# Kernel optimization log

Measured on AMD Instinct MI355X. Metric: run time of the kernel, lower is better.

## Reference

```python
import jax, jax.numpy as jnp
import numpy as np

DEPTH = 6
IN_FEATURES = 256
NUM_TREES = 256
TREE_DIM = 1
BATCH = 2048


def sparsemax(X, axis=0):
    """Full-sort sparsemax projection along `axis` (k=None path of the torch code)."""
    X = jnp.moveaxis(X, axis, -1)
    Xs = X - jnp.max(X, axis=-1, keepdims=True)
    z = -jnp.sort(-Xs, axis=-1)                      # descending sort
    cs = jnp.cumsum(z, axis=-1) - 1.0                # topk_cumsum - 1
    d = X.shape[-1]
    rho = jnp.arange(1, d + 1, dtype=X.dtype)
    support = rho * z > cs
    k = jnp.sum(support, axis=-1, keepdims=True)     # support size (int)
    tau = jnp.take_along_axis(cs, k - 1, axis=-1) / k.astype(X.dtype)
    out = jnp.maximum(Xs - tau, 0.0)
    return jnp.moveaxis(out, -1, axis)


def sparsemoid(x):
    return jnp.clip(0.5 * x + 0.5, 0.0, 1.0)


def bin_codes_1hot(depth, dtype=jnp.float32):
    idx = jnp.arange(2 ** depth)
    off = 2 ** jnp.arange(depth)
    codes = ((idx[None, :] // off[:, None]) % 2).astype(dtype)   # [depth, 2^depth]
    return jnp.stack([codes, 1.0 - codes], axis=-1)              # [depth, 2^depth, 2]


def setup_inputs() -> dict:
    key = jax.random.key(0)
    k1, k2, k3, k4, k5 = jax.random.split(key, 5)
    x = jax.random.normal(k1, (BATCH, IN_FEATURES), dtype=jnp.float32)
    response = jax.random.normal(k2, (NUM_TREES, TREE_DIM, 2 ** DEPTH), dtype=jnp.float32)
    feature_selection_logits = jax.random.uniform(k3, (IN_FEATURES, NUM_TREES, DEPTH), dtype=jnp.float32)
    feature_thresholds = 0.5 * jax.random.normal(k4, (NUM_TREES, DEPTH), dtype=jnp.float32)
    log_temperatures = jnp.zeros((NUM_TREES, DEPTH), dtype=jnp.float32)
    return {
        "x": x,
        "response": response,
        "feature_selection_logits": feature_selection_logits,
        "feature_thresholds": feature_thresholds,
        "log_temperatures": log_temperatures,
    }


def reference(x, response, feature_selection_logits, feature_thresholds, log_temperatures):
    depth = feature_thresholds.shape[-1]
    codes = bin_codes_1hot(depth, x.dtype)                          # [d, 2^d, 2]
    # sparsemax feature routing over the feature axis
    fs = sparsemax(feature_selection_logits, axis=0)                # [F, T, d]
    fv = jnp.einsum('bi,ind->bnd', x, fs)                           # [B, T, d]
    tl = (fv - feature_thresholds) * jnp.exp(-log_temperatures)     # [B, T, d]
    bins = sparsemoid(jnp.stack([-tl, tl], axis=-1))                # [B, T, d, 2]
    bin_matches = jnp.einsum('btds,dcs->btdc', bins, codes)         # [B, T, d, 2^d]
    response_weights = jnp.prod(bin_matches, axis=-2)               # [B, T, 2^d]
    out = jnp.einsum('bnd,ncd->bnc', response_weights, response)    # [B, T, C]
    return out.reshape(out.shape[0], -1)                            # flatten_output=True
```

## Files before the change

kernel.cpp:

```cpp
#include <hip/hip_runtime.h>
#include <math.h>

#define NF 256
#define NT 256
#define ND 6
#define NB 2048
#define NCOL (NT * ND)
#define NLEAF 64

typedef __attribute__((ext_vector_type(8))) short bf16x8;
typedef __attribute__((ext_vector_type(4))) float f32x4;
typedef __attribute__((ext_vector_type(8))) unsigned short u16x8;

__device__ inline unsigned short f2bf(float f) {
    unsigned u = __float_as_uint(f);
    u += 0x7fffu + ((u >> 16) & 1u);
    return (unsigned short)(u >> 16);
}
__device__ inline float bf2f(unsigned short h) {
    return __uint_as_float(((unsigned)h) << 16);
}

__global__ __launch_bounds__(256) void convert_x_kernel(
    const float* __restrict__ x,
    unsigned short* __restrict__ xh,
    unsigned short* __restrict__ xl)
{
    const int i = (blockIdx.x * 256 + threadIdx.x) * 4;
    const float4 v = *(const float4*)&x[i];
    const unsigned short h0 = f2bf(v.x), h1 = f2bf(v.y), h2 = f2bf(v.z), h3 = f2bf(v.w);
    *(ushort4*)&xh[i] = make_ushort4(h0, h1, h2, h3);
    *(ushort4*)&xl[i] = make_ushort4(f2bf(v.x - bf2f(h0)), f2bf(v.y - bf2f(h1)),
                                     f2bf(v.z - bf2f(h2)), f2bf(v.w - bf2f(h3)));
}

__global__ __launch_bounds__(256) void sparsemax_kernel(
    const float* __restrict__ fsl,
    unsigned short* __restrict__ fs_hi,
    unsigned short* __restrict__ fs_lo)
{
    __shared__ float s[NF];
    __shared__ int wk[4];
    const int col = blockIdx.x;
    const int tid = threadIdx.x;

    const float v = fsl[tid * NCOL + col];

    s[tid] = v;
    __syncthreads();
    for (int off = 128; off > 0; off >>= 1) {
        if (tid < off) s[tid] = fmaxf(s[tid], s[tid + off]);
        __syncthreads();
    }
    const float xmax = s[0];
    __syncthreads();

    const float xs = v - xmax;

    s[tid] = xs;
    __syncthreads();
    for (int k = 2; k <= NF; k <<= 1) {
        for (int j = k >> 1; j > 0; j >>= 1) {
            const int ixj = tid ^ j;
            if (ixj > tid) {
                const float a = s[tid];
                const float b = s[ixj];
                const bool desc = ((tid & k) == 0);
                if (desc ? (a < b) : (a > b)) { s[tid] = b; s[ixj] = a; }
            }
            __syncthreads();
        }
    }
    const float z = s[tid];

    for (int off = 1; off < NF; off <<= 1) {
        const float tmp = (tid >= off) ? s[tid - off] : 0.0f;
        __syncthreads();
        s[tid] += tmp;
        __syncthreads();
    }

    const bool flag = ((float)(tid + 1) * z > s[tid] - 1.0f);
    const unsigned long long m = __ballot(flag);
    if ((tid & 63) == 0) wk[tid >> 6] = __popcll(m);
    __syncthreads();
    const int k = wk[0] + wk[1] + wk[2] + wk[3];

    const float tau = (s[k - 1] - 1.0f) / (float)k;
    const float val = fmaxf(xs - tau, 0.0f);
    const unsigned short h = f2bf(val);
    fs_hi[col * NF + tid] = h;
    fs_lo[col * NF + tid] = f2bf(val - bf2f(h));
}

#define TM 64
#define TN 64
#define TK 32

__global__ __launch_bounds__(256) void gemm_mfma_kernel(
    const unsigned short* __restrict__ Ah, const unsigned short* __restrict__ Al,
    const unsigned short* __restrict__ Bh, const unsigned short* __restrict__ Bl,
    float* __restrict__ C)
{
    __shared__ unsigned short sAh[TM][TK], sAl[TM][TK];
    __shared__ unsigned short sBh[TN][TK], sBl[TN][TK];

    const int tid  = threadIdx.x;
    const int lane = tid & 63;
    const int w    = tid >> 6;
    const int wm   = w & 1;
    const int wn   = w >> 1;
    const int bm0  = blockIdx.y * TM;
    const int bn0  = blockIdx.x * TN;

    const int l15  = lane & 15;
    const int quad = lane >> 4;

    const int srow  = tid >> 2;
    const int skseg = (tid & 3) * 8;

    f32x4 acc[2][2] = {};

    for (int k0 = 0; k0 < NF; k0 += TK) {
        *(u16x8*)&sAh[srow][skseg] = *(const u16x8*)&Ah[(bm0 + srow) * NF + k0 + skseg];
        *(u16x8*)&sAl[srow][skseg] = *(const u16x8*)&Al[(bm0 + srow) * NF + k0 + skseg];
        *(u16x8*)&sBh[srow][skseg] = *(const u16x8*)&Bh[(bn0 + srow) * NF + k0 + skseg];
        *(u16x8*)&sBl[srow][skseg] = *(const u16x8*)&Bl[(bn0 + srow) * NF + k0 + skseg];
        __syncthreads();

        #pragma unroll
        for (int im = 0; im < 2; im++) {
            const bf16x8 a_h = *(const bf16x8*)&sAh[wm * 32 + im * 16 + l15][quad * 8];
            const bf16x8 a_l = *(const bf16x8*)&sAl[wm * 32 + im * 16 + l15][quad * 8];
            #pragma unroll
            for (int in = 0; in < 2; in++) {
                const bf16x8 b_h = *(const bf16x8*)&sBh[wn * 32 + in * 16 + l15][quad * 8];
                const bf16x8 b_l = *(const bf16x8*)&sBl[wn * 32 + in * 16 + l15][quad * 8];
                acc[im][in] = __builtin_amdgcn_mfma_f32_16x16x32_bf16(a_h, b_h, acc[im][in], 0, 0, 0);
                acc[im][in] = __builtin_amdgcn_mfma_f32_16x16x32_bf16(a_h, b_l, acc[im][in], 0, 0, 0);
                acc[im][in] = __builtin_amdgcn_mfma_f32_16x16x32_bf16(a_l, b_h, acc[im][in], 0, 0, 0);
            }
        }
        __syncthreads();
    }

    #pragma unroll
    for (int im = 0; im < 2; im++)
        #pragma unroll
        for (int in = 0; in < 2; in++)
            #pragma unroll
            for (int r = 0; r < 4; r++) {
                const int m = bm0 + wm * 32 + im * 16 + quad * 4 + r;
                const int n = bn0 + wn * 32 + in * 16 + l15;
                C[m * NCOL + n] = acc[im][in][r];
            }
}

__global__ __launch_bounds__(256) void tree_kernel(
    const float* __restrict__ fv,
    const float* __restrict__ thr,
    const float* __restrict__ ltemp,
    const float* __restrict__ resp,
    float* __restrict__ out)
{
    const int b = blockIdx.x;
    const int t = threadIdx.x;

    float sp[ND], sm[ND];
    #pragma unroll
    for (int d = 0; d < ND; d++) {
        const float f  = fv[b * NCOL + t * ND + d];
        const float tl = (f - thr[t * ND + d]) * expf(-ltemp[t * ND + d]);
        const float h  = 0.5f * tl;
        sp[d] = fminf(fmaxf(0.5f + h, 0.0f), 1.0f);
        sm[d] = fminf(fmaxf(0.5f - h, 0.0f), 1.0f);
    }

    float wleaf[NLEAF];
    wleaf[0] = 1.0f;
    #pragma unroll
    for (int d = 0; d < ND; d++) {
        const int half = 1 << d;
        #pragma unroll
        for (int c = 0; c < NLEAF / 2; c++) {
            if (c < half) {
                const float base = wleaf[c];
                wleaf[c + half] = base * sm[d];
                wleaf[c]        = base * sp[d];
            }
        }
    }

    float acc = 0.0f;
    #pragma unroll
    for (int c = 0; c < NLEAF; c++)
        acc = fmaf(wleaf[c], resp[t * NLEAF + c], acc);

    out[b * NT + t] = acc;
}

extern "C" void kernel_launch(void* const* d_in, const int* in_sizes, int n_in,
                              void* d_out, int out_size, void* d_ws, size_t ws_size,
                              hipStream_t stream)
{
    const float* x    = (const float*)d_in[0];
    const float* resp = (const float*)d_in[1];
    const float* fsl  = (const float*)d_in[2];
    const float* thr  = (const float*)d_in[3];
    const float* lt   = (const float*)d_in[4];
    float* out = (float*)d_out;

    float* fv = (float*)d_ws;
    unsigned short* xh    = (unsigned short*)(fv + (size_t)NB * NCOL);
    unsigned short* xl    = xh + (size_t)NB * NF;
    unsigned short* fs_hi = xl + (size_t)NB * NF;
    unsigned short* fs_lo = fs_hi + (size_t)NCOL * NF;

    convert_x_kernel<<<NB * NF / (256 * 4), 256, 0, stream>>>(x, xh, xl);
    sparsemax_kernel<<<NCOL, 256, 0, stream>>>(fsl, fs_hi, fs_lo);

    dim3 g(NCOL / TN, NB / TM);
    gemm_mfma_kernel<<<g, 256, 0, stream>>>(xh, xl, fs_hi, fs_lo, fv);

    tree_kernel<<<NB, 256, 0, stream>>>(fv, thr, lt, resp, out);
}
```

Baseline: 110.8 us.

## Fuse GEMM with tree epilogue, inline x conversion, use Michelot sparsemax

Replaces the sort-based sparsemax with a per-wavefront Michelot fixed-point iteration that handles four columns per block using shuffles. The x bf16 hi/lo split moves into the GEMM tile load. The tree evaluation becomes a GEMM epilogue working from shared memory, with N tiles widened to 96 so each tile covers 16 whole trees. This removes two kernel launches and the global round trip of the 2048x1536 feature-value matrix. In exchange it adds an iterative sparsemax whose iteration count depends on the data, and a heavier epilogue per block.

```diff
diff --git a/kernel.cpp b/kernel.cpp
--- a/kernel.cpp
+++ b/kernel.cpp
@@ -21,89 +21,84 @@
     return __uint_as_float(((unsigned)h) << 16);
 }
 
-__global__ __launch_bounds__(256) void convert_x_kernel(
-    const float* __restrict__ x,
-    unsigned short* __restrict__ xh,
-    unsigned short* __restrict__ xl)
-{
-    const int i = (blockIdx.x * 256 + threadIdx.x) * 4;
-    const float4 v = *(const float4*)&x[i];
-    const unsigned short h0 = f2bf(v.x), h1 = f2bf(v.y), h2 = f2bf(v.z), h3 = f2bf(v.w);
-    *(ushort4*)&xh[i] = make_ushort4(h0, h1, h2, h3);
-    *(ushort4*)&xl[i] = make_ushort4(f2bf(v.x - bf2f(h0)), f2bf(v.y - bf2f(h1)),
-                                     f2bf(v.z - bf2f(h2)), f2bf(v.w - bf2f(h3)));
-}
-
-__global__ __launch_bounds__(256) void sparsemax_kernel(
+__global__ __launch_bounds__(256) void sparsemax_michelot(
     const float* __restrict__ fsl,
     unsigned short* __restrict__ fs_hi,
     unsigned short* __restrict__ fs_lo)
 {
-    __shared__ float s[NF];
-    __shared__ int wk[4];
-    const int col = blockIdx.x;
-    const int tid = threadIdx.x;
-
-    const float v = fsl[tid * NCOL + col];
-
-    s[tid] = v;
-    __syncthreads();
-    for (int off = 128; off > 0; off >>= 1) {
-        if (tid < off) s[tid] = fmaxf(s[tid], s[tid + off]);
-        __syncthreads();
-    }
-    const float xmax = s[0];
-    __syncthreads();
-
-    const float xs = v - xmax;
-
-    s[tid] = xs;
-    __syncthreads();
-    for (int k = 2; k <= NF; k <<= 1) {
-        for (int j = k >> 1; j > 0; j >>= 1) {
-            const int ixj = tid ^ j;
-            if (ixj > tid) {
-                const float a = s[tid];
-                const float b = s[ixj];
-                const bool desc = ((tid & k) == 0);
-                if (desc ? (a < b) : (a > b)) { s[tid] = b; s[ixj] = a; }
-            }
-            __syncthreads();
-        }
-    }
-    const float z = s[tid];
-
-    for (int off = 1; off < NF; off <<= 1) {
-        const float tmp = (tid >= off) ? s[tid - off] : 0.0f;
-        __syncthreads();
-        s[tid] += tmp;
-        __syncthreads();
-    }
-
-    const bool flag = ((float)(tid + 1) * z > s[tid] - 1.0f);
-    const unsigned long long m = __ballot(flag);
-    if ((tid & 63) == 0) wk[tid >> 6] = __popcll(m);
-    __syncthreads();
-    const int k = wk[0] + wk[1] + wk[2] + wk[3];
-
-    const float tau = (s[k - 1] - 1.0f) / (float)k;
-    const float val = fmaxf(xs - tau, 0.0f);
-    const unsigned short h = f2bf(val);
-    fs_hi[col * NF + tid] = h;
-    fs_lo[col * NF + tid] = f2bf(val - bf2f(h));
+    const int lane = threadIdx.x & 63;
+    const int col  = blockIdx.x * 4 + (threadIdx.x >> 6);
+
+    float x[4];
+    #pragma unroll
+    for (int j = 0; j < 4; j++)
+        x[j] = fsl[(lane + 64 * j) * NCOL + col];
+
+    float mx = fmaxf(fmaxf(x[0], x[1]), fmaxf(x[2], x[3]));
+    #pragma unroll
+    for (int off = 32; off > 0; off >>= 1)
+        mx = fmaxf(mx, __shfl_xor(mx, off));
+    #pragma unroll
+    for (int j = 0; j < 4; j++) x[j] -= mx;
+
+    float s = (x[0] + x[1]) + (x[2] + x[3]);
+    #pragma unroll
+    for (int off = 32; off > 0; off >>= 1)
+        s += __shfl_xor(s, off);
+    float tau = (s - 1.0f) / 256.0f;
+
+    int prev = 256;
+    for (int it = 0; it < 64; it++) {
+        float ss = 0.0f, cc = 0.0f;
+        #pragma unroll
+        for (int j = 0; j < 4; j++)
+            if (x[j] > tau) { ss += x[j]; cc += 1.0f; }
+        #pragma unroll
+        for (int off = 32; off > 0; off >>= 1) {
+            ss += __shfl_xor(ss, off);
+            cc += __shfl_xor(cc, off);
+        }
+        const int c = (int)cc;
+        if (c == prev) break;
+        prev = c;
+        tau = (ss - 1.0f) / cc;
+    }
+
+    #pragma unroll
+    for (int j = 0; j < 4; j++) {
+        const float v = fmaxf(x[j] - tau, 0.0f);
+        const unsigned short h = f2bf(v);
+        fs_hi[col * NF + lane + 64 * j] = h;
+        fs_lo[col * NF + lane + 64 * j] = f2bf(v - bf2f(h));
+    }
 }
 
 #define TM 64
-#define TN 64
+#define TN 96
 #define TK 32
-
-__global__ __launch_bounds__(256) void gemm_mfma_kernel(
-    const unsigned short* __restrict__ Ah, const unsigned short* __restrict__ Al,
-    const unsigned short* __restrict__ Bh, const unsigned short* __restrict__ Bl,
-    float* __restrict__ C)
+#define PK (TK + 8)
+
+union SMem {
+    struct {
+        unsigned short Ah[TM][PK], Al[TM][PK];
+        unsigned short Bh[TN][PK], Bl[TN][PK];
+    } st;
+    struct {
+        float fv[TM][TN + 1];
+        float resp[16][NLEAF];
+    } ep;
+};
+
+__global__ __launch_bounds__(256) void gemm_tree_kernel(
+    const float* __restrict__ x,
+    const unsigned short* __restrict__ Bh,
+    const unsigned short* __restrict__ Bl,
+    const float* __restrict__ thr,
+    const float* __restrict__ ltemp,
+    const float* __restrict__ resp_g,
+    float* __restrict__ out)
 {
-    __shared__ unsigned short sAh[TM][TK], sAl[TM][TK];
-    __shared__ unsigned short sBh[TN][TK], sBl[TN][TK];
+    __shared__ SMem sm;
 
     const int tid  = threadIdx.x;
     const int lane = tid & 63;
@@ -112,30 +107,54 @@
     const int wn   = w >> 1;
     const int bm0  = blockIdx.y * TM;
     const int bn0  = blockIdx.x * TN;
+    const int t0   = blockIdx.x * 16;
 
     const int l15  = lane & 15;
     const int quad = lane >> 4;
 
-    const int srow  = tid >> 2;
-    const int skseg = (tid & 3) * 8;
-
-    f32x4 acc[2][2] = {};
+    const int arow  = tid >> 2;
+    const int akseg = (tid & 3) * 8;
+    const int bhalf = tid >> 7;
+    const int brow  = (tid & 127) >> 2;
+    const int bkseg = (tid & 3) * 8;
+
+    f32x4 acc[2][3] = {};
 
     for (int k0 = 0; k0 < NF; k0 += TK) {
-        *(u16x8*)&sAh[srow][skseg] = *(const u16x8*)&Ah[(bm0 + srow) * NF + k0 + skseg];
-        *(u16x8*)&sAl[srow][skseg] = *(const u16x8*)&Al[(bm0 + srow) * NF + k0 + skseg];
-        *(u16x8*)&sBh[srow][skseg] = *(const u16x8*)&Bh[(bn0 + srow) * NF + k0 + skseg];
-        *(u16x8*)&sBl[srow][skseg] = *(const u16x8*)&Bl[(bn0 + srow) * NF + k0 + skseg];
+        {
+            const float4 v0 = *(const float4*)&x[(bm0 + arow) * NF + k0 + akseg];
+            const float4 v1 = *(const float4*)&x[(bm0 + arow) * NF + k0 + akseg + 4];
+            const float vv[8] = {v0.x, v0.y, v0.z, v0.w, v1.x, v1.y, v1.z, v1.w};
+            u16x8 hi, lo;
+            #pragma unroll
+            for (int j = 0; j < 8; j++) {
+                const unsigned short h = f2bf(vv[j]);
+                hi[j] = h;
+                lo[j] = f2bf(vv[j] - bf2f(h));
+            }
+            *(u16x8*)&sm.st.Ah[arow][akseg] = hi;
+            *(u16x8*)&sm.st.Al[arow][akseg] = lo;
+        }
+        {
+            const unsigned short* __restrict__ src = bhalf ? Bl : Bh;
+            unsigned short (*dst)[PK] = bhalf ? sm.st.Bl : sm.st.Bh;
+            #pragma unroll
+            for (int c = 0; c < 3; c++) {
+                const int row = c * 32 + brow;
+                *(u16x8*)&dst[row][bkseg] =
+                    *(const u16x8*)&src[(bn0 + row) * NF + k0 + bkseg];
+            }
+        }
         __syncthreads();
 
         #pragma unroll
         for (int im = 0; im < 2; im++) {
-            const bf16x8 a_h = *(const bf16x8*)&sAh[wm * 32 + im * 16 + l15][quad * 8];
-            const bf16x8 a_l = *(const bf16x8*)&sAl[wm * 32 + im * 16 + l15][quad * 8];
-            #pragma unroll
-            for (int in = 0; in < 2; in++) {
-                const bf16x8 b_h = *(const bf16x8*)&sBh[wn * 32 + in * 16 + l15][quad * 8];
-                const bf16x8 b_l = *(const bf16x8*)&sBl[wn * 32 + in * 16 + l15][quad * 8];
+            const bf16x8 a_h = *(const bf16x8*)&sm.st.Ah[wm * 32 + im * 16 + l15][quad * 8];
+            const bf16x8 a_l = *(const bf16x8*)&sm.st.Al[wm * 32 + im * 16 + l15][quad * 8];
+            #pragma unroll
+            for (int in = 0; in < 3; in++) {
+                const bf16x8 b_h = *(const bf16x8*)&sm.st.Bh[wn * 48 + in * 16 + l15][quad * 8];
+                const bf16x8 b_l = *(const bf16x8*)&sm.st.Bl[wn * 48 + in * 16 + l15][quad * 8];
                 acc[im][in] = __builtin_amdgcn_mfma_f32_16x16x32_bf16(a_h, b_h, acc[im][in], 0, 0, 0);
                 acc[im][in] = __builtin_amdgcn_mfma_f32_16x16x32_bf16(a_h, b_l, acc[im][in], 0, 0, 0);
                 acc[im][in] = __builtin_amdgcn_mfma_f32_16x16x32_bf16(a_l, b_h, acc[im][in], 0, 0, 0);
@@ -147,56 +166,59 @@
     #pragma unroll
     for (int im = 0; im < 2; im++)
         #pragma unroll
-        for (int in = 0; in < 2; in++)
+        for (int in = 0; in < 3; in++)
             #pragma unroll
             for (int r = 0; r < 4; r++) {
-                const int m = bm0 + wm * 32 + im * 16 + quad * 4 + r;
-                const int n = bn0 + wn * 32 + in * 16 + l15;
-                C[m * NCOL + n] = acc[im][in][r];
-            }
-}
-
-__global__ __launch_bounds__(256) void tree_kernel(
-    const float* __restrict__ fv,
-    const float* __restrict__ thr,
-    const float* __restrict__ ltemp,
-    const float* __restrict__ resp,
-    float* __restrict__ out)
-{
-    const int b = blockIdx.x;
-    const int t = threadIdx.x;
-
-    float sp[ND], sm[ND];
-    #pragma unroll
-    for (int d = 0; d < ND; d++) {
-        const float f  = fv[b * NCOL + t * ND + d];
-        const float tl = (f - thr[t * ND + d]) * expf(-ltemp[t * ND + d]);
-        const float h  = 0.5f * tl;
-        sp[d] = fminf(fmaxf(0.5f + h, 0.0f), 1.0f);
-        sm[d] = fminf(fmaxf(0.5f - h, 0.0f), 1.0f);
-    }
-
-    float wleaf[NLEAF];
-    wleaf[0] = 1.0f;
-    #pragma unroll
-    for (int d = 0; d < ND; d++) {
-        const int half = 1 << d;
-        #pragma unroll
-        for (int c = 0; c < NLEAF / 2; c++) {
-            if (c < half) {
-                const float base = wleaf[c];
-                wleaf[c + half] = base * sm[d];
-                wleaf[c]        = base * sp[d];
-            }
-        }
-    }
-
-    float acc = 0.0f;
-    #pragma unroll
-    for (int c = 0; c < NLEAF; c++)
-        acc = fmaf(wleaf[c], resp[t * NLEAF + c], acc);
-
-    out[b * NT + t] = acc;
+                const int m = wm * 32 + im * 16 + quad * 4 + r;
+                const int n = wn * 48 + in * 16 + l15;
+                sm.ep.fv[m][n] = acc[im][in][r];
+            }
+    {
+        const int tr  = tid >> 4;
+        const int seg = (tid & 15) * 4;
+        *(float4*)&sm.ep.resp[tr][seg] = *(const float4*)&resp_g[(t0 + tr) * NLEAF + seg];
+    }
+    __syncthreads();
+
+    #pragma unroll
+    for (int i = 0; i < 4; i++) {
+        const int item = tid + 256 * i;
+        const int m    = item & 63;
+        const int t16  = item >> 6;
+        const int t    = t0 + t16;
+
+        float sp[ND], sn[ND];
+        #pragma unroll
+        for (int d = 0; d < ND; d++) {
+            const float f  = sm.ep.fv[m][t16 * ND + d];
+            const float tl = (f - thr[t * ND + d]) * __expf(-ltemp[t * ND + d]);
+            const float h  = 0.5f * tl;
+            sp[d] = fminf(fmaxf(0.5f + h, 0.0f), 1.0f);
+            sn[d] = fminf(fmaxf(0.5f - h, 0.0f), 1.0f);
+        }
+
+        float wleaf[NLEAF];
+        wleaf[0] = 1.0f;
+        #pragma unroll
+        for (int d = 0; d < ND; d++) {
+            const int half = 1 << d;
+            #pragma unroll
+            for (int c = 0; c < NLEAF / 2; c++) {
+                if (c < half) {
+                    const float base = wleaf[c];
+                    wleaf[c + half] = base * sn[d];
+                    wleaf[c]        = base * sp[d];
+                }
+            }
+        }
+
+        float a = 0.0f;
+        #pragma unroll
+        for (int c = 0; c < NLEAF; c++)
+            a = fmaf(wleaf[c], sm.ep.resp[t16][c], a);
+
+        out[(bm0 + m) * NT + t] = a;
+    }
 }
 
 extern "C" void kernel_launch(void* const* d_in, const int* in_sizes, int n_in,
@@ -210,17 +232,11 @@
     const float* lt   = (const float*)d_in[4];
     float* out = (float*)d_out;
 
-    float* fv = (float*)d_ws;
-    unsigned short* xh    = (unsigned short*)(fv + (size_t)NB * NCOL);
-    unsigned short* xl    = xh + (size_t)NB * NF;
-    unsigned short* fs_hi = xl + (size_t)NB * NF;
+    unsigned short* fs_hi = (unsigned short*)d_ws;
     unsigned short* fs_lo = fs_hi + (size_t)NCOL * NF;
 
-    convert_x_kernel<<<NB * NF / (256 * 4), 256, 0, stream>>>(x, xh, xl);
-    sparsemax_kernel<<<NCOL, 256, 0, stream>>>(fsl, fs_hi, fs_lo);
+    sparsemax_michelot<<<NCOL / 4, 256, 0, stream>>>(fsl, fs_hi, fs_lo);
 
     dim3 g(NCOL / TN, NB / TM);
-    gemm_mfma_kernel<<<g, 256, 0, stream>>>(xh, xl, fs_hi, fs_lo, fv);
-
-    tree_kernel<<<NB, 256, 0, stream>>>(fv, thr, lt, resp, out);
-}
+    gemm_tree_kernel<<<g, 256, 0, stream>>>(x, fs_hi, fs_lo, thr, lt, resp, out);
+}
```

Result: faster. 89.82 us (-18.9%).
